# Optimization experiments

Hardware: AMD Instinct MI355X
Metric: run time of the kernel (lower is better)

Reference implementation:

```python
import jax, jax.numpy as jnp
import numpy as np

N = 100000
F = 128
H = 4
C = 32
E = 1600000
LEAKY_ALPHA = 0.2


def setup_inputs() -> dict:
    key = jax.random.key(0)
    k1, k2, k3, k4, k5 = jax.random.split(key, 5)
    x = jax.random.normal(k1, (N, F), dtype=jnp.float32)
    edge_index = jax.random.randint(k2, (E, 2), 0, N, dtype=jnp.int64)  # cols: (source, target)
    kernel = jax.random.normal(k3, (F, H, C), dtype=jnp.float32) * 0.05
    attn_kernel_self = jax.random.normal(k4, (C, H), dtype=jnp.float32) * 0.05
    attn_kernel_neighs = jax.random.normal(k5, (C, H), dtype=jnp.float32) * 0.05
    bias = jnp.zeros((H * C,), dtype=jnp.float32)
    return {"x": x, "edge_index": edge_index, "kernel": kernel,
            "attn_kernel_self": attn_kernel_self,
            "attn_kernel_neighs": attn_kernel_neighs, "bias": bias}


def _gat_forward(x, edge_index, kernel, attn_kernel_self, attn_kernel_neighs, bias):
    n = x.shape[0]
    # add self loops: append (i, i) for every node
    loops = jnp.arange(n, dtype=edge_index.dtype)
    indices = jnp.concatenate([edge_index, jnp.stack([loops, loops], axis=1)], axis=0)
    sources, targets = indices[:, 0], indices[:, 1]

    xp = jnp.einsum('nf,fhc->nhc', x, kernel)                 # [N,H,C]
    attn_self = jnp.einsum('nhc,ch->nh', xp, attn_kernel_self)    # [N,H]
    attn_neigh = jnp.einsum('nhc,ch->nh', xp, attn_kernel_neighs)  # [N,H]

    logits = attn_self[targets] + attn_neigh[sources]          # [Etot,H]
    logits = jnp.where(logits >= 0, logits, LEAKY_ALPHA * logits)  # leaky_relu(0.2)

    # segment softmax over targets (every node has a self loop -> no empty segments)
    seg_max = jax.ops.segment_max(logits, targets, num_segments=n)
    e = jnp.exp(logits - seg_max[targets])
    seg_sum = jax.ops.segment_sum(e, targets, num_segments=n)
    alpha = e / seg_sum[targets]                               # [Etot,H]

    # weighted aggregation (dropout is identity at inference)
    msgs = alpha[..., None] * xp[sources]                      # [Etot,H,C]
    out = jax.ops.segment_sum(msgs, targets, num_segments=n)   # [N,H,C]

    out = out.reshape(n, H * C) + bias                         # concat heads + bias, linear activation
    return out, alpha[..., None]


def reference(x, edge_index, kernel, attn_kernel_self, attn_kernel_neighs, bias):
    return _gat_forward(x, edge_index, kernel, attn_kernel_self, attn_kernel_neighs, bias)
```

## Files before the change

### kernel.cpp

```cpp
#include <hip/hip_runtime.h>
#include <hip/hip_bf16.h>
#include <math.h>

#define LEAKY(x) ((x) >= 0.0f ? (x) : 0.2f * (x))
#define CHUNK 8192

typedef __attribute__((ext_vector_type(8))) short short8;
typedef __attribute__((ext_vector_type(4))) float f32x4;
typedef __attribute__((ext_vector_type(2))) int i32x2;

__device__ __forceinline__ float bf_lo(uint32_t u) { return __uint_as_float(u << 16); }
__device__ __forceinline__ float bf_hi(uint32_t u) { return __uint_as_float(u & 0xffff0000u); }
__device__ __forceinline__ uint32_t pack2(float a, float b) {
    __hip_bfloat162 h = __float22bfloat162_rn(make_float2(a, b));
    return *reinterpret_cast<uint32_t*>(&h);
}

__global__ __launch_bounds__(256) void w_prep(
    const float* __restrict__ W, uint32_t* __restrict__ Wp)
{
    const int slot = blockIdx.x * 256 + threadIdx.x;
    if (slot >= 2048) return;
    const int kb = slot >> 9;
    const int cb = (slot >> 6) & 7;
    const int l  = slot & 63;
    const int k0 = kb * 32 + (l >> 4) * 8;
    const int col = cb * 16 + (l & 15);
    uint32_t u[4];
    #pragma unroll
    for (int p = 0; p < 4; ++p) {
        const float a = W[(size_t)(k0 + 2 * p) * 128 + col];
        const float b = W[(size_t)(k0 + 2 * p + 1) * 128 + col];
        u[p] = pack2(a, b);
    }
    *(uint4*)&Wp[(size_t)slot * 4] = make_uint4(u[0], u[1], u[2], u[3]);
}

__global__ __launch_bounds__(256) void gemm_binA(
    const float* __restrict__ x, const uint32_t* __restrict__ Wp,
    const float* __restrict__ aks, const float* __restrict__ akn,
    uint32_t* __restrict__ xpb, float* __restrict__ attn_self,
    float* __restrict__ attn_nei, const int* __restrict__ ei,
    int2* __restrict__ stage, int* __restrict__ start_table,
    int* __restrict__ bucket_tot, int nc, int NB, int N, int E)
{
    __shared__ float xs[64][133];
    __shared__ int lh[512], lex[512], ss[256];
    const int t = threadIdx.x;

    if (blockIdx.x < nc) {
        const int base = blockIdx.x * CHUNK;
        const int end  = min(E, base + CHUNK);

        for (int i = t; i < 512; i += 256) lh[i] = 0;
        __syncthreads();
        for (int i = base + t; i < end; i += 256)
            atomicAdd(&lh[((const int2*)ei)[i].y >> 8], 1);
        __syncthreads();

        const int v0 = lh[2 * t], v1 = lh[2 * t + 1];
        ss[t] = v0 + v1;
        __syncthreads();
        for (int d = 1; d < 256; d <<= 1) {
            const int add = (t >= d) ? ss[t - d] : 0;
            __syncthreads();
            ss[t] += add;
            __syncthreads();
        }
        const int ex = ss[t] - v0 - v1;
        lex[2 * t] = ex;
        lex[2 * t + 1] = ex + v0;
        __syncthreads();

        const size_t cbase = (size_t)blockIdx.x * (NB + 1);
        for (int b = t; b <= NB; b += 256) start_table[cbase + b] = base + lex[b];
        for (int b = t; b < NB; b += 256)
            if (lh[b]) atomicAdd(&bucket_tot[b], lh[b]);
        __syncthreads();

        for (int i = base + t; i < end; i += 256) {
            const int2 e2 = ((const int2*)ei)[i];
            const int slot = atomicAdd(&lex[e2.y >> 8], 1);
            stage[base + slot] = e2;
        }
        return;
    }

    const int blk = blockIdx.x - nc;
    const int w  = t >> 6;
    const int l  = t & 63;
    const int nb = blk * 64;

    const int row  = nb + w * 16 + (l & 15);
    const int rowc = min(row, N - 1);
    const int kg   = (l >> 4) * 8;
    const float* xrow = x + (size_t)rowc * 128 + kg;

    f32x4 acc[8] = {};
    #pragma unroll
    for (int kb = 0; kb < 4; ++kb) {
        const float4 x0 = *(const float4*)(xrow + kb * 32);
        const float4 x1 = *(const float4*)(xrow + kb * 32 + 4);
        union { short8 s; uint32_t u[4]; } A;
        A.u[0] = pack2(x0.x, x0.y); A.u[1] = pack2(x0.z, x0.w);
        A.u[2] = pack2(x1.x, x1.y); A.u[3] = pack2(x1.z, x1.w);
        #pragma unroll
        for (int cb = 0; cb < 8; ++cb) {
            union { short8 s; uint4 u; } B;
            B.u = *(const uint4*)&Wp[(((size_t)(kb * 8 + cb)) * 64 + l) * 4];
            acc[cb] = __builtin_amdgcn_mfma_f32_16x16x32_bf16(A.s, B.s, acc[cb], 0, 0, 0);
        }
    }

    const int r0 = (l >> 4) * 4;
    const int cl = l & 15;
    #pragma unroll
    for (int cb = 0; cb < 8; ++cb)
        #pragma unroll
        for (int r = 0; r < 4; ++r)
            xs[w * 16 + r0 + r][cb * 16 + cl] = acc[cb][r];
    __syncthreads();

    #pragma unroll
    for (int i = 0; i < 16; ++i) {
        const int idx = t + i * 256;
        const int n = idx >> 6, q = idx & 63;
        const int gn = nb + n;
        if (gn < N)
            xpb[(size_t)gn * 64 + q] = pack2(xs[n][2 * q], xs[n][2 * q + 1]);
    }

    {
        const int n = t & 63, h = t >> 6;
        const int gn = nb + n;
        if (gn < N) {
            float sv = 0.0f, sn = 0.0f;
            #pragma unroll
            for (int c = 0; c < 32; ++c) {
                const float v = xs[n][h * 32 + c];
                sv = fmaf(v, aks[c * 4 + h], sv);
                sn = fmaf(v, akn[c * 4 + h], sn);
            }
            attn_self[(size_t)gn * 4 + h] = sv;
            attn_nei [(size_t)gn * 4 + h] = sn;
        }
    }
}

__global__ __launch_bounds__(256) void binB(
    const int2* __restrict__ stage, const int* __restrict__ start_table,
    const int* __restrict__ bucket_tot, int* __restrict__ offsets,
    int* __restrict__ csr_src, int nc, int NB, int N, int E)
{
    __shared__ int s0[256], cum[257], ss[256], lcnt[256], lcur[256], red[256];
    const int t  = threadIdx.x;
    const int b  = blockIdx.x;
    const int lo = b << 8;
    const int nn = min(N, lo + 256) - lo;

    int part = 0;
    for (int i = t; i < b; i += 256) part += bucket_tot[i];
    red[t] = part;
    if (t == 0 && b == 0) offsets[N] = E;

    int len = 0;
    if (t < nc) {
        const size_t cb = (size_t)t * (NB + 1);
        const int a0 = start_table[cb + b];
        s0[t] = a0;
        len   = start_table[cb + b + 1] - a0;
    }
    ss[t] = len;
    lcnt[t] = 0;
    __syncthreads();
    for (int d = 128; d > 0; d >>= 1) {
        if (t < d) red[t] += red[t + d];
        __syncthreads();
    }
    const int boff = red[0];
    for (int d = 1; d < 256; d <<= 1) {
        const int add = (t >= d) ? ss[t - d] : 0;
        __syncthreads();
        ss[t] += add;
        __syncthreads();
    }
    if (t == 0) cum[0] = 0;
    cum[t + 1] = ss[t];
    __syncthreads();
    const int T = cum[nc];

    for (int g = t; g < T; g += 256) {
        int loc = 0, hic = nc - 1;
        while (loc < hic) {
            const int mid = (loc + hic + 1) >> 1;
            if (cum[mid] <= g) loc = mid; else hic = mid - 1;
        }
        const int2 e = stage[s0[loc] + (g - cum[loc])];
        atomicAdd(&lcnt[e.y - lo], 1);
    }
    __syncthreads();

    const int v = lcnt[t];
    ss[t] = v;
    __syncthreads();
    for (int d = 1; d < 256; d <<= 1) {
        const int add = (t >= d) ? ss[t - d] : 0;
        __syncthreads();
        ss[t] += add;
        __syncthreads();
    }
    const int nodeoff = boff + ss[t] - v;
    lcur[t] = nodeoff;
    if (t < nn) offsets[lo + t] = nodeoff;
    __syncthreads();

    for (int g = t; g < T; g += 256) {
        int loc = 0, hic = nc - 1;
        while (loc < hic) {
            const int mid = (loc + hic + 1) >> 1;
            if (cum[mid] <= g) loc = mid; else hic = mid - 1;
        }
        const int2 e = stage[s0[loc] + (g - cum[loc])];
        const int slot = atomicAdd(&lcur[e.y - lo], 1);
        csr_src[slot] = e.x;
    }
}

__global__ __launch_bounds__(256) void aggregate(
    const int* __restrict__ csr_src, const int* __restrict__ offsets,
    const uint32_t* __restrict__ xpb, const float* __restrict__ attn_self,
    const float* __restrict__ attn_nei, const float* __restrict__ bias,
    float* __restrict__ out, float* __restrict__ alpha_out,
    float* __restrict__ inv_arr, int N, int E)
{
    const int lane = threadIdx.x & 63;
    int node = blockIdx.x * 4 + (threadIdx.x >> 6);
    if (node >= N) return;
    node = __builtin_amdgcn_readfirstlane(node);

    const int hL = lane >> 4;
    const int c0 = 2 * lane;

    const float asH = attn_self[(size_t)node * 4 + hL];
    const float anH = attn_nei [(size_t)node * 4 + hL];
    const float eS  = __expf(LEAKY(asH + anH));
    float sumE = eS;
    const uint32_t uS = xpb[(size_t)node * 64 + lane];
    float acc0 = eS * bf_lo(uS), acc1 = eS * bf_hi(uS);

    const int off0 = __builtin_amdgcn_readfirstlane(offsets[node]);
    const int deg  = __builtin_amdgcn_readfirstlane(offsets[node + 1]) - off0;
    const int* srcp = csr_src + off0;

    for (int j = 0; j < deg; j += 8) {
        int s[8];
        #pragma unroll
        for (int k = 0; k < 8; ++k) s[k] = srcp[min(j + k, deg - 1)];
        float a[8];
        #pragma unroll
        for (int k = 0; k < 8; ++k) a[k] = attn_nei[(size_t)s[k] * 4 + hL];
        uint32_t u[8];
        #pragma unroll
        for (int k = 0; k < 8; ++k) u[k] = xpb[(size_t)s[k] * 64 + lane];
        #pragma unroll
        for (int k = 0; k < 8; ++k) {
            const float v = (j + k < deg) ? __expf(LEAKY(asH + a[k])) : 0.0f;
            sumE += v;
            acc0 = fmaf(v, bf_lo(u[k]), acc0);
            acc1 = fmaf(v, bf_hi(u[k]), acc1);
        }
    }

    const float inv = 1.0f / sumE;
    union { float2 f; unsigned long long u; } o;
    o.f = make_float2(fmaf(acc0, inv, bias[c0]), fmaf(acc1, inv, bias[c0 + 1]));
    __builtin_nontemporal_store(o.u,
        (unsigned long long*)&out[(size_t)node * 128 + c0]);
    if ((lane & 15) == 0) {
        inv_arr[(size_t)node * 4 + hL] = inv;
        __builtin_nontemporal_store(eS * inv,
            &alpha_out[(size_t)(E + node) * 4 + hL]);
    }
}

__global__ __launch_bounds__(256) void alpha_kernel(
    const int* __restrict__ ei, const float* __restrict__ attn_self,
    const float* __restrict__ attn_nei, const float* __restrict__ inv_arr,
    float* __restrict__ alpha_out, int E)
{
    const int i = blockIdx.x * 256 + threadIdx.x;
    if (i >= E) return;
    const i32x2 e2 = __builtin_nontemporal_load((const i32x2*)ei + i);
    const int src = e2.x, tgt = e2.y;
    const float4 as4 = *(const float4*)&attn_self[(size_t)tgt * 4];
    const float4 an4 = *(const float4*)&attn_nei[(size_t)src * 4];
    const float4 iv4 = *(const float4*)&inv_arr[(size_t)tgt * 4];
    f32x4 a;
    a.x = __expf(LEAKY(as4.x + an4.x)) * iv4.x;
    a.y = __expf(LEAKY(as4.y + an4.y)) * iv4.y;
    a.z = __expf(LEAKY(as4.z + an4.z)) * iv4.z;
    a.w = __expf(LEAKY(as4.w + an4.w)) * iv4.w;
    __builtin_nontemporal_store(a, (f32x4*)&alpha_out[(size_t)i * 4]);
}

extern "C" void kernel_launch(void* const* d_in, const int* in_sizes, int n_in,
                              void* d_out, int out_size, void* d_ws, size_t ws_size,
                              hipStream_t stream)
{
    const float* x    = (const float*)d_in[0];
    const int*   ei   = (const int*)d_in[1];
    const float* W    = (const float*)d_in[2];
    const float* aks  = (const float*)d_in[3];
    const float* akn  = (const float*)d_in[4];
    const float* bias = (const float*)d_in[5];

    const int N  = in_sizes[0] / 128;
    const int E  = in_sizes[1] / 2;
    const int NB = (N + 255) >> 8;
    const int nc = (E + CHUNK - 1) / CHUNK;

    float* out       = (float*)d_out;
    float* alpha_out = out + (size_t)N * 128;
    int2* stage      = (int2*)alpha_out;

    char* p = (char*)d_ws;
    auto alloc = [&](size_t bytes) {
        char* r = p;
        p += (bytes + 255) & ~(size_t)255;
        return r;
    };
    uint32_t* xpb       = (uint32_t*)alloc((size_t)N * 64 * 4);
    uint32_t* Wp        = (uint32_t*)alloc((size_t)2048 * 16);
    float* attn_self    = (float*)alloc((size_t)N * 4 * 4);
    float* attn_nei     = (float*)alloc((size_t)N * 4 * 4);
    float* inv_arr      = (float*)alloc((size_t)N * 4 * 4);
    int*   offsets      = (int*)alloc((size_t)(N + 1) * 4);
    int*   csr_src      = (int*)alloc((size_t)E * 4);
    int*   bucket_tot   = (int*)alloc((size_t)NB * 4);
    int*   start_table  = (int*)alloc((size_t)nc * (NB + 1) * 4);

    hipMemsetAsync(bucket_tot, 0, (size_t)NB * 4, stream);

    w_prep<<<8, 256, 0, stream>>>(W, Wp);
    gemm_binA<<<nc + (N + 63) / 64, 256, 0, stream>>>(
        x, Wp, aks, akn, xpb, attn_self, attn_nei,
        ei, stage, start_table, bucket_tot, nc, NB, N, E);
    binB<<<NB, 256, 0, stream>>>(stage, start_table, bucket_tot, offsets,
                                 csr_src, nc, NB, N, E);
    aggregate<<<(N + 3) / 4, 256, 0, stream>>>(csr_src, offsets, xpb,
                                               attn_self, attn_nei, bias, out,
                                               alpha_out, inv_arr, N, E);
    alpha_kernel<<<(E + 255) / 256, 256, 0, stream>>>(ei, attn_self, attn_nei,
                                                      inv_arr, alpha_out, E);
}
```

Before: 192.7 us.

## Regroup CSR build stages into fewer launches and drop bucket_tot atomics

Weight packing is merged into the edge-bucketing kernel, and the bucket-scatter pass (binB) is merged into the GEMM kernel, so the pipeline runs one memset and two launches fewer. Each bucket's global offset is now derived from start_table (a0 - chunk base, summed over chunks), which removes the global atomics into bucket_tot. The GEMM tile is staged in LDS as bf16 instead of fp32, shrinking shared memory, and x is read with nontemporal loads. Attention logits are now computed from bf16-rounded xp rather than fp32, which slightly changes numerics.

```diff
diff --git a/kernel.cpp b/kernel.cpp
--- a/kernel.cpp
+++ b/kernel.cpp
@@ -16,77 +16,158 @@
     return *reinterpret_cast<uint32_t*>(&h);
 }
 
-__global__ __launch_bounds__(256) void w_prep(
-    const float* __restrict__ W, uint32_t* __restrict__ Wp)
-{
-    const int slot = blockIdx.x * 256 + threadIdx.x;
-    if (slot >= 2048) return;
-    const int kb = slot >> 9;
-    const int cb = (slot >> 6) & 7;
-    const int l  = slot & 63;
-    const int k0 = kb * 32 + (l >> 4) * 8;
-    const int col = cb * 16 + (l & 15);
-    uint32_t u[4];
-    #pragma unroll
-    for (int p = 0; p < 4; ++p) {
-        const float a = W[(size_t)(k0 + 2 * p) * 128 + col];
-        const float b = W[(size_t)(k0 + 2 * p + 1) * 128 + col];
-        u[p] = pack2(a, b);
-    }
-    *(uint4*)&Wp[(size_t)slot * 4] = make_uint4(u[0], u[1], u[2], u[3]);
-}
-
-__global__ __launch_bounds__(256) void gemm_binA(
+__global__ __launch_bounds__(256) void binA_wprep(
+    const int* __restrict__ ei, int2* __restrict__ stage,
+    int* __restrict__ start_table, const float* __restrict__ W,
+    uint32_t* __restrict__ Wp, int nc, int NB, int E)
+{
+    __shared__ int lh[512], lex[512], ss[256];
+    const int t = threadIdx.x;
+
+    if (blockIdx.x >= nc) {
+        const int slot = (blockIdx.x - nc) * 256 + t;
+        if (slot >= 2048) return;
+        const int kb = slot >> 9;
+        const int cb = (slot >> 6) & 7;
+        const int l  = slot & 63;
+        const int k0 = kb * 32 + (l >> 4) * 8;
+        const int col = cb * 16 + (l & 15);
+        uint32_t u[4];
+        #pragma unroll
+        for (int p = 0; p < 4; ++p) {
+            const float a = W[(size_t)(k0 + 2 * p) * 128 + col];
+            const float b = W[(size_t)(k0 + 2 * p + 1) * 128 + col];
+            u[p] = pack2(a, b);
+        }
+        *(uint4*)&Wp[(size_t)slot * 4] = make_uint4(u[0], u[1], u[2], u[3]);
+        return;
+    }
+
+    const int base = blockIdx.x * CHUNK;
+    const int end  = min(E, base + CHUNK);
+
+    for (int i = t; i < 512; i += 256) lh[i] = 0;
+    __syncthreads();
+    for (int i = base + t; i < end; i += 256)
+        atomicAdd(&lh[((const int2*)ei)[i].y >> 8], 1);
+    __syncthreads();
+
+    const int v0 = lh[2 * t], v1 = lh[2 * t + 1];
+    ss[t] = v0 + v1;
+    __syncthreads();
+    for (int d = 1; d < 256; d <<= 1) {
+        const int add = (t >= d) ? ss[t - d] : 0;
+        __syncthreads();
+        ss[t] += add;
+        __syncthreads();
+    }
+    const int ex = ss[t] - v0 - v1;
+    lex[2 * t] = ex;
+    lex[2 * t + 1] = ex + v0;
+    __syncthreads();
+
+    const size_t cbase = (size_t)blockIdx.x * (NB + 1);
+    for (int b = t; b <= NB; b += 256) start_table[cbase + b] = base + lex[b];
+    __syncthreads();
+
+    for (int i = base + t; i < end; i += 256) {
+        const int2 e2 = ((const int2*)ei)[i];
+        const int slot = atomicAdd(&lex[e2.y >> 8], 1);
+        stage[base + slot] = e2;
+    }
+}
+
+__global__ __launch_bounds__(256) void gemm_binB(
     const float* __restrict__ x, const uint32_t* __restrict__ Wp,
     const float* __restrict__ aks, const float* __restrict__ akn,
     uint32_t* __restrict__ xpb, float* __restrict__ attn_self,
-    float* __restrict__ attn_nei, const int* __restrict__ ei,
-    int2* __restrict__ stage, int* __restrict__ start_table,
-    int* __restrict__ bucket_tot, int nc, int NB, int N, int E)
-{
-    __shared__ float xs[64][133];
-    __shared__ int lh[512], lex[512], ss[256];
+    float* __restrict__ attn_nei, const int2* __restrict__ stage,
+    const int* __restrict__ start_table, int* __restrict__ offsets,
+    int* __restrict__ csr_src, int nc, int NB, int N, int E)
+{
+    __shared__ __align__(16) char smem[16896];
     const int t = threadIdx.x;
 
-    if (blockIdx.x < nc) {
-        const int base = blockIdx.x * CHUNK;
-        const int end  = min(E, base + CHUNK);
-
-        for (int i = t; i < 512; i += 256) lh[i] = 0;
-        __syncthreads();
-        for (int i = base + t; i < end; i += 256)
-            atomicAdd(&lh[((const int2*)ei)[i].y >> 8], 1);
-        __syncthreads();
-
-        const int v0 = lh[2 * t], v1 = lh[2 * t + 1];
-        ss[t] = v0 + v1;
-        __syncthreads();
+    if (blockIdx.x < NB) {
+        int* s0   = (int*)smem;
+        int* cum  = s0 + 256;
+        int* ss   = cum + 257;
+        int* lcnt = ss + 256;
+        int* lcur = lcnt + 256;
+        int* red  = lcur + 256;
+        const int b  = blockIdx.x;
+        const int lo = b << 8;
+        const int nn = min(N, lo + 256) - lo;
+
+        int part = 0, len = 0;
+        if (t < nc) {
+            const size_t cb = (size_t)t * (NB + 1);
+            const int a0 = start_table[cb + b];
+            s0[t] = a0;
+            len   = start_table[cb + b + 1] - a0;
+            part  = a0 - t * CHUNK;
+        }
+        ss[t] = len;
+        lcnt[t] = 0;
+        red[t] = part;
+        if (t == 0 && b == 0) offsets[N] = E;
+        __syncthreads();
+        for (int d = 128; d > 0; d >>= 1) {
+            if (t < d) red[t] += red[t + d];
+            __syncthreads();
+        }
+        const int boff = red[0];
         for (int d = 1; d < 256; d <<= 1) {
             const int add = (t >= d) ? ss[t - d] : 0;
             __syncthreads();
             ss[t] += add;
             __syncthreads();
         }
-        const int ex = ss[t] - v0 - v1;
-        lex[2 * t] = ex;
-        lex[2 * t + 1] = ex + v0;
-        __syncthreads();
-
-        const size_t cbase = (size_t)blockIdx.x * (NB + 1);
-        for (int b = t; b <= NB; b += 256) start_table[cbase + b] = base + lex[b];
-        for (int b = t; b < NB; b += 256)
-            if (lh[b]) atomicAdd(&bucket_tot[b], lh[b]);
-        __syncthreads();
-
-        for (int i = base + t; i < end; i += 256) {
-            const int2 e2 = ((const int2*)ei)[i];
-            const int slot = atomicAdd(&lex[e2.y >> 8], 1);
-            stage[base + slot] = e2;
+        if (t == 0) cum[0] = 0;
+        cum[t + 1] = ss[t];
+        __syncthreads();
+        const int T = cum[nc];
+
+        for (int g = t; g < T; g += 256) {
+            int loc = 0, hic = nc - 1;
+            while (loc < hic) {
+                const int mid = (loc + hic + 1) >> 1;
+                if (cum[mid] <= g) loc = mid; else hic = mid - 1;
+            }
+            const int2 e = stage[s0[loc] + (g - cum[loc])];
+            atomicAdd(&lcnt[e.y - lo], 1);
+        }
+        __syncthreads();
+
+        const int v = lcnt[t];
+        ss[t] = v;
+        __syncthreads();
+        for (int d = 1; d < 256; d <<= 1) {
+            const int add = (t >= d) ? ss[t - d] : 0;
+            __syncthreads();
+            ss[t] += add;
+            __syncthreads();
+        }
+        const int nodeoff = boff + ss[t] - v;
+        lcur[t] = nodeoff;
+        if (t < nn) offsets[lo + t] = nodeoff;
+        __syncthreads();
+
+        for (int g = t; g < T; g += 256) {
+            int loc = 0, hic = nc - 1;
+            while (loc < hic) {
+                const int mid = (loc + hic + 1) >> 1;
+                if (cum[mid] <= g) loc = mid; else hic = mid - 1;
+            }
+            const int2 e = stage[s0[loc] + (g - cum[loc])];
+            const int slot = atomicAdd(&lcur[e.y - lo], 1);
+            csr_src[slot] = e.x;
         }
         return;
     }
 
-    const int blk = blockIdx.x - nc;
+    ushort (*xs)[132] = (ushort(*)[132])smem;
+    const int blk = blockIdx.x - NB;
     const int w  = t >> 6;
     const int l  = t & 63;
     const int nb = blk * 64;
@@ -99,8 +180,8 @@
     f32x4 acc[8] = {};
     #pragma unroll
     for (int kb = 0; kb < 4; ++kb) {
-        const float4 x0 = *(const float4*)(xrow + kb * 32);
-        const float4 x1 = *(const float4*)(xrow + kb * 32 + 4);
+        const f32x4 x0 = __builtin_nontemporal_load((const f32x4*)(xrow + kb * 32));
+        const f32x4 x1 = __builtin_nontemporal_load((const f32x4*)(xrow + kb * 32 + 4));
         union { short8 s; uint32_t u[4]; } A;
         A.u[0] = pack2(x0.x, x0.y); A.u[1] = pack2(x0.z, x0.w);
         A.u[2] = pack2(x1.x, x1.y); A.u[3] = pack2(x1.z, x1.w);
@@ -118,7 +199,8 @@
     for (int cb = 0; cb < 8; ++cb)
         #pragma unroll
         for (int r = 0; r < 4; ++r)
-            xs[w * 16 + r0 + r][cb * 16 + cl] = acc[cb][r];
+            xs[w * 16 + r0 + r][cb * 16 + cl] =
+                (ushort)(pack2(acc[cb][r], 0.0f) & 0xffffu);
     __syncthreads();
 
     #pragma unroll
@@ -127,7 +209,7 @@
         const int n = idx >> 6, q = idx & 63;
         const int gn = nb + n;
         if (gn < N)
-            xpb[(size_t)gn * 64 + q] = pack2(xs[n][2 * q], xs[n][2 * q + 1]);
+            xpb[(size_t)gn * 64 + q] = *(const uint32_t*)&xs[n][2 * q];
     }
 
     {
@@ -137,92 +219,13 @@
             float sv = 0.0f, sn = 0.0f;
             #pragma unroll
             for (int c = 0; c < 32; ++c) {
-                const float v = xs[n][h * 32 + c];
+                const float v = __uint_as_float((uint32_t)xs[n][h * 32 + c] << 16);
                 sv = fmaf(v, aks[c * 4 + h], sv);
                 sn = fmaf(v, akn[c * 4 + h], sn);
             }
             attn_self[(size_t)gn * 4 + h] = sv;
             attn_nei [(size_t)gn * 4 + h] = sn;
         }
-    }
-}
-
-__global__ __launch_bounds__(256) void binB(
-    const int2* __restrict__ stage, const int* __restrict__ start_table,
-    const int* __restrict__ bucket_tot, int* __restrict__ offsets,
-    int* __restrict__ csr_src, int nc, int NB, int N, int E)
-{
-    __shared__ int s0[256], cum[257], ss[256], lcnt[256], lcur[256], red[256];
-    const int t  = threadIdx.x;
-    const int b  = blockIdx.x;
-    const int lo = b << 8;
-    const int nn = min(N, lo + 256) - lo;
-
-    int part = 0;
-    for (int i = t; i < b; i += 256) part += bucket_tot[i];
-    red[t] = part;
-    if (t == 0 && b == 0) offsets[N] = E;
-
-    int len = 0;
-    if (t < nc) {
-        const size_t cb = (size_t)t * (NB + 1);
-        const int a0 = start_table[cb + b];
-        s0[t] = a0;
-        len   = start_table[cb + b + 1] - a0;
-    }
-    ss[t] = len;
-    lcnt[t] = 0;
-    __syncthreads();
-    for (int d = 128; d > 0; d >>= 1) {
-        if (t < d) red[t] += red[t + d];
-        __syncthreads();
-    }
-    const int boff = red[0];
-    for (int d = 1; d < 256; d <<= 1) {
-        const int add = (t >= d) ? ss[t - d] : 0;
-        __syncthreads();
-        ss[t] += add;
-        __syncthreads();
-    }
-    if (t == 0) cum[0] = 0;
-    cum[t + 1] = ss[t];
-    __syncthreads();
-    const int T = cum[nc];
-
-    for (int g = t; g < T; g += 256) {
-        int loc = 0, hic = nc - 1;
-        while (loc < hic) {
-            const int mid = (loc + hic + 1) >> 1;
-            if (cum[mid] <= g) loc = mid; else hic = mid - 1;
-        }
-        const int2 e = stage[s0[loc] + (g - cum[loc])];
-        atomicAdd(&lcnt[e.y - lo], 1);
-    }
-    __syncthreads();
-
-    const int v = lcnt[t];
-    ss[t] = v;
-    __syncthreads();
-    for (int d = 1; d < 256; d <<= 1) {
-        const int add = (t >= d) ? ss[t - d] : 0;
-        __syncthreads();
-        ss[t] += add;
-        __syncthreads();
-    }
-    const int nodeoff = boff + ss[t] - v;
-    lcur[t] = nodeoff;
-    if (t < nn) offsets[lo + t] = nodeoff;
-    __syncthreads();
-
-    for (int g = t; g < T; g += 256) {
-        int loc = 0, hic = nc - 1;
-        while (loc < hic) {
-            const int mid = (loc + hic + 1) >> 1;
-            if (cum[mid] <= g) loc = mid; else hic = mid - 1;
-        }
-        const int2 e = stage[s0[loc] + (g - cum[loc])];
-        const int slot = atomicAdd(&lcur[e.y - lo], 1);
-        csr_src[slot] = e.x;
     }
 }
 
@@ -336,17 +339,13 @@
     float* inv_arr      = (float*)alloc((size_t)N * 4 * 4);
     int*   offsets      = (int*)alloc((size_t)(N + 1) * 4);
     int*   csr_src      = (int*)alloc((size_t)E * 4);
-    int*   bucket_tot   = (int*)alloc((size_t)NB * 4);
     int*   start_table  = (int*)alloc((size_t)nc * (NB + 1) * 4);
 
-    hipMemsetAsync(bucket_tot, 0, (size_t)NB * 4, stream);
-
-    w_prep<<<8, 256, 0, stream>>>(W, Wp);
-    gemm_binA<<<nc + (N + 63) / 64, 256, 0, stream>>>(
+    binA_wprep<<<nc + 8, 256, 0, stream>>>(ei, stage, start_table, W, Wp,
+                                           nc, NB, E);
+    gemm_binB<<<NB + (N + 63) / 64, 256, 0, stream>>>(
         x, Wp, aks, akn, xpb, attn_self, attn_nei,
-        ei, stage, start_table, bucket_tot, nc, NB, N, E);
-    binB<<<NB, 256, 0, stream>>>(stage, start_table, bucket_tot, offsets,
-                                 csr_src, nc, NB, N, E);
+        stage, start_table, offsets, csr_src, nc, NB, N, E);
     aggregate<<<(N + 3) / 4, 256, 0, stream>>>(csr_src, offsets, xpb,
                                                attn_self, attn_nei, bias, out,
                                                alpha_out, inv_arr, N, E);
```

Measured after the change: 182.4 us. 1.06x faster.
